# Performance work log

Hardware: AMD Instinct MI355X
Metric: run time of the kernel (lower is better)

Reference implementation:

```python
import jax, jax.numpy as jnp
import numpy as np

BETA = 0.9
TH = 1.0  # snn.Leaky default threshold
SPARSITY = 0.5


@jax.custom_vjp
def spike(x):
    # Heaviside spike; surrogate (atan, alpha=2) gradient as in snntorch default
    return (x > 0).astype(x.dtype)

def _spike_fwd(x):
    return spike(x), x

def _spike_bwd(x, g):
    return (g / (1.0 + (jnp.pi * x) ** 2),)

spike.defvjp(_spike_fwd, _spike_bwd)


def setup_inputs() -> dict:
    key = jax.random.key(0)
    ks = jax.random.split(key, 6)
    T, B, NIN, NH, NOUT = 50, 512, 784, 1000, 10

    def mk_w(k, o, i):
        k1, k2 = jax.random.split(k)
        w = jax.random.normal(k1, (o, i), jnp.float32) * (1.0 / np.sqrt(i))
        mask = (jax.random.uniform(k2, (o, i)) > SPARSITY).astype(jnp.float32)
        return w * mask

    x = jax.random.normal(ks[0], (T, B, NIN), jnp.float32)
    return dict(
        x=x,
        W0=mk_w(ks[1], NH, NIN), b0=jnp.zeros((NH,), jnp.float32),
        W1=mk_w(ks[2], NH, NH), b1=jnp.zeros((NH,), jnp.float32),
        W2=mk_w(ks[3], NH, NH), b2=jnp.zeros((NH,), jnp.float32),
        W3=mk_w(ks[4], NOUT, NH), b3=jnp.zeros((NOUT,), jnp.float32),
    )


def reference(x, W0, b0, W1, b1, W2, b2, W3, b3):
    params = ((W0, b0), (W1, b1), (W2, b2), (W3, b3))
    B = x.shape[1]
    mems0 = tuple(jnp.zeros((B, W.shape[0]), x.dtype) for W, _ in params)

    def step(mems, xt):
        inp = xt
        new_mems, spks = [], []
        for (W, b), m in zip(params, mems):
            cur = inp @ W.T + b
            # snntorch Leaky (reset_mechanism='subtract'):
            # reset from previous mem (detached), then mem = beta*mem + I - reset*th
            reset = jax.lax.stop_gradient((m > TH).astype(x.dtype))
            m_new = BETA * m + cur - reset * TH
            s = spike(m_new - TH)
            new_mems.append(m_new)
            spks.append(s)
            inp = s
        return tuple(new_mems), (tuple(spks), tuple(new_mems))

    _, (spk_rec, mem_rec) = jax.lax.scan(step, mems0, x)
    # spk_rec/mem_rec: tuples of [T, B, dim] arrays per layer
    return (*spk_rec, *mem_rec)
```

## Files before the change

### kernel.cpp

```cpp
#include <hip/hip_runtime.h>


typedef int int4v  __attribute__((ext_vector_type(4)));
typedef int int16v __attribute__((ext_vector_type(16)));

#define XSCALE 68719476736.0
#define WSCALE 1099511627776.0
#define MT 25600

__global__ void wsplit_i8(const float* __restrict__ W, signed char* __restrict__ out,
                          int Nreal, int Npad, int K, int Kpad)
{
    int idx = blockIdx.x * blockDim.x + threadIdx.x;
    int total = Npad * Kpad;
    if (idx >= total) return;
    int n = idx / Kpad, k = idx - n * Kpad;
    long long v = 0;
    if (n < Nreal && k < K) v = __double2ll_rn((double)W[(size_t)n * K + k] * WSCALE);
    size_t plane = (size_t)total;
#pragma unroll
    for (int p = 0; p < 4; ++p) {
        int d = (int)(v & 255); if (d > 127) d -= 256;
        out[p * plane + idx] = (signed char)d;
        v = (v - d) >> 8;
    }
    out[4 * plane + idx] = (signed char)v;
}

__global__ void xsplit_all(const float* __restrict__ x, signed char* __restrict__ out)
{
    int idx = blockIdx.x * blockDim.x + threadIdx.x;
    if (idx >= MT * 832) return;
    int row = idx / 832, k = idx - row * 832;
    long long v = 0;
    if (k < 784) v = __double2ll_rn((double)x[(size_t)row * 784 + k] * XSCALE);
    const size_t plane = (size_t)MT * 832;
    signed char* o = out + idx;
#pragma unroll
    for (int p = 0; p < 4; ++p) {
        int d = (int)(v & 255); if (d > 127) d -= 256;
        o[p * plane] = (signed char)d;
        v = (v - d) >> 8;
    }
    o[4 * plane] = (signed char)v;
}

__device__ __forceinline__ void xcd_map(int bid, int mtiles, int& m_tile, int& n_tile)
{
    int k = bid & 7, j = bid >> 3;
    n_tile = (k & 1) * 8 + (j & 7);
    m_tile = (k >> 1) * (mtiles >> 2) + (j >> 3);
}

template<int NA, int KP, int CS, bool SWZ>
__global__ __launch_bounds__(256)
void gemm32(const signed char* __restrict__ Ap, size_t planeA,
            const signed char* __restrict__ Wp, size_t planeW,
            double* __restrict__ curout, int mtiles)
{
    __shared__ __align__(16) signed char Wld[5 * 64 * 80];
    __shared__ __align__(16) signed char Ald[NA * 64 * 80];
    constexpr int NIT = KP / 64;

    const int tid = threadIdx.x;
    const int l   = tid & 63;
    const int w   = tid >> 6;
    const int wm  = (w & 1) * 32;
    const int wn  = (w >> 1) * 32;
    const int r32 = l & 31;
    const int h   = l >> 5;

    int bm, bn;
    if constexpr (SWZ) {
        int m_tile, n_tile;
        xcd_map(blockIdx.x, mtiles, m_tile, n_tile);
        bm = m_tile * 64; bn = n_tile * 64;
    } else {
        bm = blockIdx.y * 64; bn = blockIdx.x * 64;
    }

    const int srow = tid >> 2;
    const int sc   = (tid & 3) * 16;

    const signed char* ag = Ap + (size_t)(bm + srow) * KP + sc;
    const signed char* wg = Wp + (size_t)(bn + srow) * KP + sc;

    int4v Ar[NA], Wr[5];
#pragma unroll
    for (int p = 0; p < 5; ++p)  Wr[p] = *(const int4v*)(wg + p * planeW);
#pragma unroll
    for (int p = 0; p < NA; ++p) Ar[p] = *(const int4v*)(ag + p * planeA);

    int16v acc[5];
#pragma unroll
    for (int s = 0; s < 5; ++s)
#pragma unroll
        for (int r = 0; r < 16; ++r) acc[s][r] = 0;

    for (int it = 0; it < NIT; ++it) {
        __syncthreads();
#pragma unroll
        for (int p = 0; p < 5; ++p)
            *(int4v*)&Wld[(p * 64 + srow) * 80 + sc] = Wr[p];
#pragma unroll
        for (int p = 0; p < NA; ++p)
            *(int4v*)&Ald[(p * 64 + srow) * 80 + sc] = Ar[p];
        __syncthreads();

        if (it + 1 < NIT) {
            int kb = (it + 1) * 64;
#pragma unroll
            for (int p = 0; p < 5; ++p)
                Wr[p] = *(const int4v*)(wg + kb + p * planeW);
#pragma unroll
            for (int p = 0; p < NA; ++p)
                Ar[p] = *(const int4v*)(ag + kb + p * planeA);
        }

#pragma unroll
        for (int k2 = 0; k2 < 2; ++k2) {
            const int off = k2 * 32 + 16 * h;
            if constexpr (NA == 5) {
                int4v af[5], bq[5];
#pragma unroll
                for (int p = 0; p < 5; ++p)
                    af[p] = *(const int4v*)&Ald[(p * 64 + wm + r32) * 80 + off];
#pragma unroll
                for (int q = 0; q < 5; ++q)
                    bq[q] = *(const int4v*)&Wld[(q * 64 + wn + r32) * 80 + off];
#pragma unroll
                for (int q = 0; q < 5; ++q)
#pragma unroll
                    for (int p = 0; p < 5; ++p)
                        if (p + q >= 4)
                            acc[p + q - 4] = __builtin_amdgcn_mfma_i32_32x32x32_i8(
                                af[p], bq[q], acc[p + q - 4], 0, 0, 0);
            } else {
                int4v a0 = *(const int4v*)&Ald[(wm + r32) * 80 + off];
#pragma unroll
                for (int q = 0; q < 5; ++q) {
                    int4v bq = *(const int4v*)&Wld[(q * 64 + wn + r32) * 80 + off];
                    acc[q] = __builtin_amdgcn_mfma_i32_32x32x32_i8(a0, bq, acc[q], 0, 0, 0);
                }
            }
        }
    }

    const int col = bn + wn + r32;
    if (col < CS) {
#pragma unroll
        for (int reg = 0; reg < 16; ++reg) {
            int row = bm + wm + (reg & 3) + 8 * (reg >> 2) + 4 * h;
            double v = (double)acc[4][reg];
            v = v * 256.0 + (double)acc[3][reg];
            v = v * 256.0 + (double)acc[2][reg];
            v = v * 256.0 + (double)acc[1][reg];
            v = v * 256.0 + (double)acc[0][reg];
            curout[(size_t)row * CS + col] = v * (NA == 5 ? 0x1p-44 : 0x1p-40);
        }
    }
}

template<int KP>
__global__ __launch_bounds__(256)
void gemm32w(const signed char* __restrict__ Asp,
             const signed char* __restrict__ Wp, size_t planeW,
             double* __restrict__ curout, int mtiles)
{
    __shared__ __align__(16) signed char Wld[5 * 64 * 80];
    __shared__ __align__(16) signed char Ald[128 * 80];
    constexpr int NIT = KP / 64;

    const int tid = threadIdx.x;
    const int l   = tid & 63;
    const int w   = tid >> 6;
    const int wm  = (w & 1) * 64;
    const int wn  = (w >> 1) * 32;
    const int r32 = l & 31;
    const int h   = l >> 5;

    int m_tile, n_tile;
    xcd_map(blockIdx.x, mtiles, m_tile, n_tile);
    const int bm = m_tile * 128;
    const int bn = n_tile * 64;

    const int srA = tid >> 1;
    const int scA = (tid & 1) * 32;
    const int srW = tid >> 2;
    const int scW = (tid & 3) * 16;

    const signed char* ag = Asp + (size_t)(bm + srA) * KP + scA;
    const signed char* wg = Wp  + (size_t)(bn + srW) * KP + scW;

    int4v Ar0 = *(const int4v*)(ag);
    int4v Ar1 = *(const int4v*)(ag + 16);
    int4v Wr[5];
#pragma unroll
    for (int p = 0; p < 5; ++p) Wr[p] = *(const int4v*)(wg + p * planeW);

    int16v acc[2][5];
#pragma unroll
    for (int mi = 0; mi < 2; ++mi)
#pragma unroll
        for (int s = 0; s < 5; ++s)
#pragma unroll
            for (int r = 0; r < 16; ++r) acc[mi][s][r] = 0;

    for (int it = 0; it < NIT; ++it) {
        __syncthreads();
#pragma unroll
        for (int p = 0; p < 5; ++p)
            *(int4v*)&Wld[(p * 64 + srW) * 80 + scW] = Wr[p];
        *(int4v*)&Ald[srA * 80 + scA]      = Ar0;
        *(int4v*)&Ald[srA * 80 + scA + 16] = Ar1;
        __syncthreads();

        if (it + 1 < NIT) {
            int kb = (it + 1) * 64;
            Ar0 = *(const int4v*)(ag + kb);
            Ar1 = *(const int4v*)(ag + kb + 16);
#pragma unroll
            for (int p = 0; p < 5; ++p)
                Wr[p] = *(const int4v*)(wg + kb + p * planeW);
        }

#pragma unroll
        for (int k2 = 0; k2 < 2; ++k2) {
            const int off = k2 * 32 + 16 * h;
            int4v bq[5];
#pragma unroll
            for (int q = 0; q < 5; ++q)
                bq[q] = *(const int4v*)&Wld[(q * 64 + wn + r32) * 80 + off];
#pragma unroll
            for (int mi = 0; mi < 2; ++mi) {
                int4v a0 = *(const int4v*)&Ald[(wm + mi * 32 + r32) * 80 + off];
#pragma unroll
                for (int q = 0; q < 5; ++q)
                    acc[mi][q] = __builtin_amdgcn_mfma_i32_32x32x32_i8(
                        a0, bq[q], acc[mi][q], 0, 0, 0);
            }
        }
    }

    const int col = bn + wn + r32;
#pragma unroll
    for (int mi = 0; mi < 2; ++mi)
#pragma unroll
        for (int reg = 0; reg < 16; ++reg) {
            int row = bm + wm + mi * 32 + (reg & 3) + 8 * (reg >> 2) + 4 * h;
            double v = (double)acc[mi][4][reg];
            v = v * 256.0 + (double)acc[mi][3][reg];
            v = v * 256.0 + (double)acc[mi][2][reg];
            v = v * 256.0 + (double)acc[mi][1][reg];
            v = v * 256.0 + (double)acc[mi][0][reg];
            curout[(size_t)row * 1024 + col] = v * 0x1p-40;
        }
}

__global__ __launch_bounds__(256)
void if_update(const double* __restrict__ cur, const float* __restrict__ bias,
               float* __restrict__ spk, float* __restrict__ mem,
               signed char* __restrict__ spk_i8)
{
    int idx = blockIdx.x * blockDim.x + threadIdx.x;
    if (idx >= 512 * 512) return;
    int row = idx >> 9, col = (idx & 511) * 2;
    if (col >= 1000) {
        for (int t = 0; t < 50; ++t)
            *(short*)&spk_i8[((size_t)t * 512 + row) * 1024 + col] = 0;
        return;
    }
    double mp0 = 0.0, mp1 = 0.0;
    double bs0 = (double)bias[col], bs1 = (double)bias[col + 1];
    for (int t = 0; t < 50; ++t) {
        double2 c = *(const double2*)&cur[((size_t)t * 512 + row) * 1024 + col];
        double rst0 = (mp0 > 1.0) ? 1.0 : 0.0;
        double rst1 = (mp1 > 1.0) ? 1.0 : 0.0;
        double mn0 = 0.9 * mp0 + (c.x + bs0) - rst0;
        double mn1 = 0.9 * mp1 + (c.y + bs1) - rst1;
        int s0 = (mn0 > 1.0) ? 1 : 0;
        int s1 = (mn1 > 1.0) ? 1 : 0;
        size_t o = ((size_t)t * 512 + row) * 1000 + col;
        *(float2*)&spk[o] = make_float2((float)s0, (float)s1);
        *(float2*)&mem[o] = make_float2((float)mn0, (float)mn1);
        *(short*)&spk_i8[((size_t)t * 512 + row) * 1024 + col] =
            (short)(s0 | (s1 << 8));
        mp0 = mn0; mp1 = mn1;
    }
}

__global__ __launch_bounds__(256)
void if3_kernel(const double* __restrict__ cur3, const float* __restrict__ bias,
                float* __restrict__ spk3, float* __restrict__ mem3)
{
    int idx = blockIdx.x * blockDim.x + threadIdx.x;
    if (idx >= 5120) return;
    int brow = idx / 10, col = idx - brow * 10;
    double bs = (double)bias[col];
    double mp = 0.0;
    for (int t = 0; t < 50; ++t) {
        double c   = cur3[((size_t)t * 512 + brow) * 16 + col] + bs;
        double rst = (mp > 1.0) ? 1.0 : 0.0;
        double mn  = 0.9 * mp + c - rst;
        size_t o   = (size_t)t * 5120 + (size_t)brow * 10 + col;
        spk3[o] = (mn > 1.0) ? 1.0f : 0.0f;
        mem3[o] = (float)mn;
        mp = mn;
    }
}

extern "C" void kernel_launch(void* const* d_in, const int* in_sizes, int n_in,
                              void* d_out, int out_size, void* d_ws, size_t ws_size,
                              hipStream_t stream)
{
    const float* x  = (const float*)d_in[0];
    const float* W0 = (const float*)d_in[1];
    const float* b0 = (const float*)d_in[2];
    const float* W1 = (const float*)d_in[3];
    const float* b1 = (const float*)d_in[4];
    const float* W2 = (const float*)d_in[5];
    const float* b2 = (const float*)d_in[6];
    const float* W3 = (const float*)d_in[7];
    const float* b3 = (const float*)d_in[8];
    float* out = (float*)d_out;

    const int T = 50;
    const size_t LNH = (size_t)512 * 1000;
    const size_t LNO = (size_t)512 * 10;

    float* spk0 = out;
    float* spk1 = spk0 + (size_t)T * LNH;
    float* spk2 = spk1 + (size_t)T * LNH;
    float* spk3 = spk2 + (size_t)T * LNH;
    float* mem0 = spk3 + (size_t)T * LNO;
    float* mem1 = mem0 + (size_t)T * LNH;
    float* mem2 = mem1 + (size_t)T * LNH;
    float* mem3 = mem2 + (size_t)T * LNH;

    double* cur = (double*)d_ws;
    signed char* W0d = (signed char*)(cur + (size_t)MT * 1024);
    signed char* W1d = W0d + (size_t)5 * 1024 * 832;
    signed char* W2d = W1d + (size_t)5 * 1024 * 1024;
    signed char* W3d = W2d + (size_t)5 * 1024 * 1024;
    signed char* xsb = W3d + (size_t)5 * 64 * 1024;
    signed char* sp0 = xsb + (size_t)5 * MT * 832;
    signed char* sp1 = sp0 + (size_t)MT * 1024;
    signed char* sp2 = sp1 + (size_t)MT * 1024;

    wsplit_i8<<<(1024 * 832  + 255) / 256, 256, 0, stream>>>(W0, W0d, 1000, 1024, 784,  832);
    wsplit_i8<<<(1024 * 1024 + 255) / 256, 256, 0, stream>>>(W1, W1d, 1000, 1024, 1000, 1024);
    wsplit_i8<<<(1024 * 1024 + 255) / 256, 256, 0, stream>>>(W2, W2d, 1000, 1024, 1000, 1024);
    wsplit_i8<<<(64 * 1024   + 255) / 256, 256, 0, stream>>>(W3, W3d, 10,   64,   1000, 1024);

    xsplit_all<<<(MT * 832 + 255) / 256, 256, 0, stream>>>(x, xsb);

    const size_t plA0 = (size_t)MT * 832;
    const size_t plW0 = (size_t)1024 * 832;
    const size_t plWH = (size_t)1024 * 1024;
    const size_t plW3 = (size_t)64 * 1024;

    dim3 blk(256);

    gemm32<5, 832, 1024, true><<<6400, blk, 0, stream>>>(xsb, plA0, W0d, plW0, cur, 400);
    if_update<<<1024, 256, 0, stream>>>(cur, b0, spk0, mem0, sp0);
    gemm32w<1024><<<3200, blk, 0, stream>>>(sp0, W1d, plWH, cur, 200);
    if_update<<<1024, 256, 0, stream>>>(cur, b1, spk1, mem1, sp1);
    gemm32w<1024><<<3200, blk, 0, stream>>>(sp1, W2d, plWH, cur, 200);
    if_update<<<1024, 256, 0, stream>>>(cur, b2, spk2, mem2, sp2);
    gemm32<1, 1024, 16, false><<<dim3(1, 400), blk, 0, stream>>>(sp2, 0, W3d, plW3, cur, 0);
    if3_kernel<<<20, 256, 0, stream>>>(cur, b3, spk3, mem3);
}
```

Measured before the change: 1.079 ms.

## Switch layer GEMMs to 16x16x64 int8 MFMA with 512-thread 128x64 tiles

Replaces the 32x32x32 int8 MFMA GEMMs for layers 0-2 with new kernels built on the 16x16x64 int8 MFMA. They use 512-thread blocks covering 128x64 output tiles with 8 waves, each wave owning 64x16. Layer 0 moves from 64x64 tiles (6400 blocks) to 128x64 tiles (3200 blocks), which raises A/W reuse per block. The aim is higher MFMA throughput and better operand reuse, at the cost of more LDS reads per MFMA, a larger LDS footprint and different register pressure.

```diff
diff --git a/kernel.cpp b/kernel.cpp
--- a/kernel.cpp
+++ b/kernel.cpp
@@ -52,11 +52,186 @@
     m_tile = (k >> 1) * (mtiles >> 2) + (j >> 3);
 }
 
-template<int NA, int KP, int CS, bool SWZ>
+__global__ __launch_bounds__(512)
+void gemm16_l0(const signed char* __restrict__ Ap, size_t planeA,
+               const signed char* __restrict__ Wp, size_t planeW,
+               double* __restrict__ curout)
+{
+    constexpr int KP = 832, NIT = 13;
+    __shared__ __align__(16) signed char Ald[5 * 128 * 80];
+    __shared__ __align__(16) signed char Wld[5 * 64 * 80];
+
+    const int tid = threadIdx.x;
+    const int l   = tid & 63;
+    const int w   = tid >> 6;
+    const int mh  = (w & 1) * 64;
+    const int wn  = (w >> 1) * 16;
+    const int fr  = l & 15;
+    const int g   = l >> 4;
+
+    int m_tile, n_tile;
+    xcd_map(blockIdx.x, 200, m_tile, n_tile);
+    const int bm = m_tile * 128, bn = n_tile * 64;
+
+    const int srA = tid >> 2, scA = (tid & 3) * 16;
+    const int srW = tid >> 3, scW = (tid & 7) * 8;
+
+    const signed char* ag = Ap + (size_t)(bm + srA) * KP + scA;
+    const signed char* wg = Wp + (size_t)(bn + srW) * KP + scW;
+
+    int4v Ar[5];
+    unsigned long long Wr[5];
+#pragma unroll
+    for (int p = 0; p < 5; ++p) {
+        Ar[p] = *(const int4v*)(ag + p * planeA);
+        Wr[p] = *(const unsigned long long*)(wg + p * planeW);
+    }
+
+    int4v acc[5][4];
+#pragma unroll
+    for (int b = 0; b < 5; ++b)
+#pragma unroll
+        for (int mi = 0; mi < 4; ++mi) acc[b][mi] = (int4v){0, 0, 0, 0};
+
+    for (int it = 0; it < NIT; ++it) {
+        __syncthreads();
+#pragma unroll
+        for (int p = 0; p < 5; ++p) {
+            *(int4v*)&Ald[(p * 128 + srA) * 80 + scA] = Ar[p];
+            *(unsigned long long*)&Wld[(p * 64 + srW) * 80 + scW] = Wr[p];
+        }
+        __syncthreads();
+
+        if (it + 1 < NIT) {
+            int kb = (it + 1) * 64;
+#pragma unroll
+            for (int p = 0; p < 5; ++p) {
+                Ar[p] = *(const int4v*)(ag + kb + p * planeA);
+                Wr[p] = *(const unsigned long long*)(wg + kb + p * planeW);
+            }
+        }
+
+        int4v bq[5];
+#pragma unroll
+        for (int q = 0; q < 5; ++q)
+            bq[q] = *(const int4v*)&Wld[(q * 64 + wn + fr) * 80 + 16 * g];
+#pragma unroll
+        for (int mi = 0; mi < 4; ++mi) {
+#pragma unroll
+            for (int p = 0; p < 5; ++p) {
+                int4v af = *(const int4v*)&Ald[(p * 128 + mh + mi * 16 + fr) * 80 + 16 * g];
+#pragma unroll
+                for (int q = 0; q < 5; ++q)
+                    if (p + q >= 4)
+                        acc[p + q - 4][mi] = __builtin_amdgcn_mfma_i32_16x16x64_i8(
+                            af, bq[q], acc[p + q - 4][mi], 0, 0, 0);
+            }
+        }
+    }
+
+    const int col = bn + wn + fr;
+#pragma unroll
+    for (int mi = 0; mi < 4; ++mi)
+#pragma unroll
+        for (int r = 0; r < 4; ++r) {
+            int row = bm + mh + mi * 16 + 4 * g + r;
+            double v = (double)acc[4][mi][r];
+            v = v * 256.0 + (double)acc[3][mi][r];
+            v = v * 256.0 + (double)acc[2][mi][r];
+            v = v * 256.0 + (double)acc[1][mi][r];
+            v = v * 256.0 + (double)acc[0][mi][r];
+            curout[(size_t)row * 1024 + col] = v * 0x1p-44;
+        }
+}
+
+__global__ __launch_bounds__(512)
+void gemm16_sp(const signed char* __restrict__ Asp,
+               const signed char* __restrict__ Wp, size_t planeW,
+               double* __restrict__ curout)
+{
+    constexpr int KP = 1024, NIT = 16;
+    __shared__ __align__(16) signed char Ald[128 * 80];
+    __shared__ __align__(16) signed char Wld[5 * 64 * 80];
+
+    const int tid = threadIdx.x;
+    const int l   = tid & 63;
+    const int w   = tid >> 6;
+    const int mh  = (w & 1) * 64;
+    const int wn  = (w >> 1) * 16;
+    const int fr  = l & 15;
+    const int g   = l >> 4;
+
+    int m_tile, n_tile;
+    xcd_map(blockIdx.x, 200, m_tile, n_tile);
+    const int bm = m_tile * 128, bn = n_tile * 64;
+
+    const int srA = tid >> 2, scA = (tid & 3) * 16;
+    const int srW = tid >> 3, scW = (tid & 7) * 8;
+
+    const signed char* ag = Asp + (size_t)(bm + srA) * KP + scA;
+    const signed char* wg = Wp  + (size_t)(bn + srW) * KP + scW;
+
+    int4v Ar = *(const int4v*)ag;
+    unsigned long long Wr[5];
+#pragma unroll
+    for (int p = 0; p < 5; ++p) Wr[p] = *(const unsigned long long*)(wg + p * planeW);
+
+    int4v acc[5][4];
+#pragma unroll
+    for (int s = 0; s < 5; ++s)
+#pragma unroll
+        for (int mi = 0; mi < 4; ++mi) acc[s][mi] = (int4v){0, 0, 0, 0};
+
+    for (int it = 0; it < NIT; ++it) {
+        __syncthreads();
+        *(int4v*)&Ald[srA * 80 + scA] = Ar;
+#pragma unroll
+        for (int p = 0; p < 5; ++p)
+            *(unsigned long long*)&Wld[(p * 64 + srW) * 80 + scW] = Wr[p];
+        __syncthreads();
+
+        if (it + 1 < NIT) {
+            int kb = (it + 1) * 64;
+            Ar = *(const int4v*)(ag + kb);
+#pragma unroll
+            for (int p = 0; p < 5; ++p)
+                Wr[p] = *(const unsigned long long*)(wg + kb + p * planeW);
+        }
+
+        int4v bq[5];
+#pragma unroll
+        for (int q = 0; q < 5; ++q)
+            bq[q] = *(const int4v*)&Wld[(q * 64 + wn + fr) * 80 + 16 * g];
+#pragma unroll
+        for (int mi = 0; mi < 4; ++mi) {
+            int4v af = *(const int4v*)&Ald[(mh + mi * 16 + fr) * 80 + 16 * g];
+#pragma unroll
+            for (int q = 0; q < 5; ++q)
+                acc[q][mi] = __builtin_amdgcn_mfma_i32_16x16x64_i8(
+                    af, bq[q], acc[q][mi], 0, 0, 0);
+        }
+    }
+
+    const int col = bn + wn + fr;
+#pragma unroll
+    for (int mi = 0; mi < 4; ++mi)
+#pragma unroll
+        for (int r = 0; r < 4; ++r) {
+            int row = bm + mh + mi * 16 + 4 * g + r;
+            double v = (double)acc[4][mi][r];
+            v = v * 256.0 + (double)acc[3][mi][r];
+            v = v * 256.0 + (double)acc[2][mi][r];
+            v = v * 256.0 + (double)acc[1][mi][r];
+            v = v * 256.0 + (double)acc[0][mi][r];
+            curout[(size_t)row * 1024 + col] = v * 0x1p-40;
+        }
+}
+
+template<int NA, int KP, int CS>
 __global__ __launch_bounds__(256)
 void gemm32(const signed char* __restrict__ Ap, size_t planeA,
             const signed char* __restrict__ Wp, size_t planeW,
-            double* __restrict__ curout, int mtiles)
+            double* __restrict__ curout)
 {
     __shared__ __align__(16) signed char Wld[5 * 64 * 80];
     __shared__ __align__(16) signed char Ald[NA * 64 * 80];
@@ -70,14 +245,8 @@
     const int r32 = l & 31;
     const int h   = l >> 5;
 
-    int bm, bn;
-    if constexpr (SWZ) {
-        int m_tile, n_tile;
-        xcd_map(blockIdx.x, mtiles, m_tile, n_tile);
-        bm = m_tile * 64; bn = n_tile * 64;
-    } else {
-        bm = blockIdx.y * 64; bn = blockIdx.x * 64;
-    }
+    const int bm = blockIdx.y * 64;
+    const int bn = blockIdx.x * 64;
 
     const int srow = tid >> 2;
     const int sc   = (tid & 3) * 16;
@@ -120,28 +289,11 @@
 #pragma unroll
         for (int k2 = 0; k2 < 2; ++k2) {
             const int off = k2 * 32 + 16 * h;
-            if constexpr (NA == 5) {
-                int4v af[5], bq[5];
-#pragma unroll
-                for (int p = 0; p < 5; ++p)
-                    af[p] = *(const int4v*)&Ald[(p * 64 + wm + r32) * 80 + off];
-#pragma unroll
-                for (int q = 0; q < 5; ++q)
-                    bq[q] = *(const int4v*)&Wld[(q * 64 + wn + r32) * 80 + off];
-#pragma unroll
-                for (int q = 0; q < 5; ++q)
-#pragma unroll
-                    for (int p = 0; p < 5; ++p)
-                        if (p + q >= 4)
-                            acc[p + q - 4] = __builtin_amdgcn_mfma_i32_32x32x32_i8(
-                                af[p], bq[q], acc[p + q - 4], 0, 0, 0);
-            } else {
-                int4v a0 = *(const int4v*)&Ald[(wm + r32) * 80 + off];
-#pragma unroll
-                for (int q = 0; q < 5; ++q) {
-                    int4v bq = *(const int4v*)&Wld[(q * 64 + wn + r32) * 80 + off];
-                    acc[q] = __builtin_amdgcn_mfma_i32_32x32x32_i8(a0, bq, acc[q], 0, 0, 0);
-                }
+            int4v a0 = *(const int4v*)&Ald[(wm + r32) * 80 + off];
+#pragma unroll
+            for (int q = 0; q < 5; ++q) {
+                int4v bq = *(const int4v*)&Wld[(q * 64 + wn + r32) * 80 + off];
+                acc[q] = __builtin_amdgcn_mfma_i32_32x32x32_i8(a0, bq, acc[q], 0, 0, 0);
             }
         }
     }
@@ -156,105 +308,9 @@
             v = v * 256.0 + (double)acc[2][reg];
             v = v * 256.0 + (double)acc[1][reg];
             v = v * 256.0 + (double)acc[0][reg];
-            curout[(size_t)row * CS + col] = v * (NA == 5 ? 0x1p-44 : 0x1p-40);
-        }
-    }
-}
-
-template<int KP>
-__global__ __launch_bounds__(256)
-void gemm32w(const signed char* __restrict__ Asp,
-             const signed char* __restrict__ Wp, size_t planeW,
-             double* __restrict__ curout, int mtiles)
-{
-    __shared__ __align__(16) signed char Wld[5 * 64 * 80];
-    __shared__ __align__(16) signed char Ald[128 * 80];
-    constexpr int NIT = KP / 64;
-
-    const int tid = threadIdx.x;
-    const int l   = tid & 63;
-    const int w   = tid >> 6;
-    const int wm  = (w & 1) * 64;
-    const int wn  = (w >> 1) * 32;
-    const int r32 = l & 31;
-    const int h   = l >> 5;
-
-    int m_tile, n_tile;
-    xcd_map(blockIdx.x, mtiles, m_tile, n_tile);
-    const int bm = m_tile * 128;
-    const int bn = n_tile * 64;
-
-    const int srA = tid >> 1;
-    const int scA = (tid & 1) * 32;
-    const int srW = tid >> 2;
-    const int scW = (tid & 3) * 16;
-
-    const signed char* ag = Asp + (size_t)(bm + srA) * KP + scA;
-    const signed char* wg = Wp  + (size_t)(bn + srW) * KP + scW;
-
-    int4v Ar0 = *(const int4v*)(ag);
-    int4v Ar1 = *(const int4v*)(ag + 16);
-    int4v Wr[5];
-#pragma unroll
-    for (int p = 0; p < 5; ++p) Wr[p] = *(const int4v*)(wg + p * planeW);
-
-    int16v acc[2][5];
-#pragma unroll
-    for (int mi = 0; mi < 2; ++mi)
-#pragma unroll
-        for (int s = 0; s < 5; ++s)
-#pragma unroll
-            for (int r = 0; r < 16; ++r) acc[mi][s][r] = 0;
-
-    for (int it = 0; it < NIT; ++it) {
-        __syncthreads();
-#pragma unroll
-        for (int p = 0; p < 5; ++p)
-            *(int4v*)&Wld[(p * 64 + srW) * 80 + scW] = Wr[p];
-        *(int4v*)&Ald[srA * 80 + scA]      = Ar0;
-        *(int4v*)&Ald[srA * 80 + scA + 16] = Ar1;
-        __syncthreads();
-
-        if (it + 1 < NIT) {
-            int kb = (it + 1) * 64;
-            Ar0 = *(const int4v*)(ag + kb);
-            Ar1 = *(const int4v*)(ag + kb + 16);
-#pragma unroll
-            for (int p = 0; p < 5; ++p)
-                Wr[p] = *(const int4v*)(wg + kb + p * planeW);
-        }
-
-#pragma unroll
-        for (int k2 = 0; k2 < 2; ++k2) {
-            const int off = k2 * 32 + 16 * h;
-            int4v bq[5];
-#pragma unroll
-            for (int q = 0; q < 5; ++q)
-                bq[q] = *(const int4v*)&Wld[(q * 64 + wn + r32) * 80 + off];
-#pragma unroll
-            for (int mi = 0; mi < 2; ++mi) {
-                int4v a0 = *(const int4v*)&Ald[(wm + mi * 32 + r32) * 80 + off];
-#pragma unroll
-                for (int q = 0; q < 5; ++q)
-                    acc[mi][q] = __builtin_amdgcn_mfma_i32_32x32x32_i8(
-                        a0, bq[q], acc[mi][q], 0, 0, 0);
-            }
-        }
-    }
-
-    const int col = bn + wn + r32;
-#pragma unroll
-    for (int mi = 0; mi < 2; ++mi)
-#pragma unroll
-        for (int reg = 0; reg < 16; ++reg) {
-            int row = bm + wm + mi * 32 + (reg & 3) + 8 * (reg >> 2) + 4 * h;
-            double v = (double)acc[mi][4][reg];
-            v = v * 256.0 + (double)acc[mi][3][reg];
-            v = v * 256.0 + (double)acc[mi][2][reg];
-            v = v * 256.0 + (double)acc[mi][1][reg];
-            v = v * 256.0 + (double)acc[mi][0][reg];
-            curout[(size_t)row * 1024 + col] = v * 0x1p-40;
-        }
+            curout[(size_t)row * CS + col] = v * 0x1p-40;
+        }
+    }
 }
 
 __global__ __launch_bounds__(256)
@@ -359,14 +415,12 @@
     const size_t plWH = (size_t)1024 * 1024;
     const size_t plW3 = (size_t)64 * 1024;
 
-    dim3 blk(256);
-
-    gemm32<5, 832, 1024, true><<<6400, blk, 0, stream>>>(xsb, plA0, W0d, plW0, cur, 400);
+    gemm16_l0<<<3200, 512, 0, stream>>>(xsb, plA0, W0d, plW0, cur);
     if_update<<<1024, 256, 0, stream>>>(cur, b0, spk0, mem0, sp0);
-    gemm32w<1024><<<3200, blk, 0, stream>>>(sp0, W1d, plWH, cur, 200);
+    gemm16_sp<<<3200, 512, 0, stream>>>(sp0, W1d, plWH, cur);
     if_update<<<1024, 256, 0, stream>>>(cur, b1, spk1, mem1, sp1);
-    gemm32w<1024><<<3200, blk, 0, stream>>>(sp1, W2d, plWH, cur, 200);
+    gemm16_sp<<<3200, 512, 0, stream>>>(sp1, W2d, plWH, cur);
     if_update<<<1024, 256, 0, stream>>>(cur, b2, spk2, mem2, sp2);
-    gemm32<1, 1024, 16, false><<<dim3(1, 400), blk, 0, stream>>>(sp2, 0, W3d, plW3, cur, 0);
+    gemm32<1, 1024, 16><<<dim3(1, 400), 256, 0, stream>>>(sp2, 0, W3d, plW3, cur);
     if3_kernel<<<20, 256, 0, stream>>>(cur, b3, spk3, mem3);
 }
```

New measurement: 1.219 ms. +13.0%, slower.
